# Kernel tuning notes

Hardware: AMD Instinct MI355X
Metric: run time of the kernel (lower is better)

## Reference

```python
import jax, jax.numpy as jnp
import numpy as np

EMBED_DIM = 768
NUM_HEADS = 12
HEAD_DIM = EMBED_DIM // NUM_HEADS
SCALE = HEAD_DIM ** -0.5


def setup_inputs() -> dict:
    key = jax.random.key(0)
    ks = jax.random.split(key, 9)
    s = EMBED_DIM ** -0.5
    x = jax.random.normal(ks[0], (16, 1024, EMBED_DIM), dtype=jnp.float32)
    Wq = jax.random.normal(ks[1], (EMBED_DIM, EMBED_DIM), dtype=jnp.float32) * s
    bq = jax.random.normal(ks[2], (EMBED_DIM,), dtype=jnp.float32) * 0.01
    Wk = jax.random.normal(ks[3], (EMBED_DIM, EMBED_DIM), dtype=jnp.float32) * s
    bk = jax.random.normal(ks[4], (EMBED_DIM,), dtype=jnp.float32) * 0.01
    Wv = jax.random.normal(ks[5], (EMBED_DIM, EMBED_DIM), dtype=jnp.float32) * s
    bv = jax.random.normal(ks[6], (EMBED_DIM,), dtype=jnp.float32) * 0.01
    Wo = jax.random.normal(ks[7], (EMBED_DIM, EMBED_DIM), dtype=jnp.float32) * s
    bo = jax.random.normal(ks[8], (EMBED_DIM,), dtype=jnp.float32) * 0.01
    return {"x": x, "Wq": Wq, "bq": bq, "Wk": Wk, "bk": bk,
            "Wv": Wv, "bv": bv, "Wo": Wo, "bo": bo}


def _split_heads(t):
    # [b, n, h*d] -> [b, h, n, d]
    b, n, _ = t.shape
    return t.reshape(b, n, NUM_HEADS, HEAD_DIM).transpose(0, 2, 1, 3)


def reference(x, Wq, bq, Wk, bk, Wv, bv, Wo, bo):
    # Linear projections (torch Linear: y = x @ W.T + b; W here stored as [out,in])
    Q = _split_heads(x @ Wq.T + bq)
    K = _split_heads(x @ Wk.T + bk)
    V = _split_heads(x @ Wv.T + bv)
    attn = jnp.einsum('bhid,bhjd->bhij', Q, K) * SCALE
    attention = jax.nn.softmax(attn, axis=-1)
    out = jnp.einsum('bhij,bhjd->bhid', attention, V)
    b, h, n, d = out.shape
    out = out.transpose(0, 2, 1, 3).reshape(b, n, h * d)
    return out @ Wo.T + bo
```

## Files before the change

### kernel.cpp

```cpp
#include <hip/hip_runtime.h>

typedef __attribute__((ext_vector_type(8))) short bf16x8;
typedef __attribute__((ext_vector_type(4))) float f32x4;

#define EMBED  768
#define NHEADS 12
#define HDIM   64
#define SEQ    1024
#define BATCH  16
#define MTOT   (BATCH * SEQ)
#define SCALE  0.125f
#define MSHIFT 11.0f
#define SEXP   0.18033688011112042f
#define MEXP   15.869645544856504f

__device__ __forceinline__ unsigned short f2bf(float f) {
  unsigned u = __float_as_uint(f);
  u += 0x7fffu + ((u >> 16) & 1u);
  return (unsigned short)(u >> 16);
}

__device__ __forceinline__ unsigned cvtpk(float lo, float hi) {
  unsigned r;
  asm("v_cvt_pk_bf16_f32 %0, %1, %2" : "=v"(r) : "v"(lo), "v"(hi));
  return r;
}

__device__ __forceinline__ float exp2v(float x) {
  return __builtin_amdgcn_exp2f(x);
}

__device__ __forceinline__ void gld_lds16(const unsigned short* g, unsigned short* l) {
  __builtin_amdgcn_global_load_lds(
      (const __attribute__((address_space(1))) unsigned int*)g,
      (__attribute__((address_space(3))) unsigned int*)l, 16, 0, 0);
}

__global__ void cvt_kernel(const float* __restrict__ in,
                           unsigned short* __restrict__ out, int n) {
  int i = (blockIdx.x * blockDim.x + threadIdx.x) * 4;
  if (i >= n) return;
  float4 v = *(const float4*)(in + i);
  ushort4 o;
  o.x = f2bf(v.x); o.y = f2bf(v.y); o.z = f2bf(v.z); o.w = f2bf(v.w);
  *(ushort4*)(out + i) = o;
}

__global__ void cvt4_kernel(const float* __restrict__ a, const float* __restrict__ b,
                            const float* __restrict__ c, const float* __restrict__ d,
                            unsigned short* __restrict__ oa, unsigned short* __restrict__ ob,
                            unsigned short* __restrict__ oc, unsigned short* __restrict__ od,
                            int n) {
  const int sel = blockIdx.y;
  const float* in = (sel == 0) ? a : (sel == 1) ? b : (sel == 2) ? c : d;
  unsigned short* out = (sel == 0) ? oa : (sel == 1) ? ob : (sel == 2) ? oc : od;
  int i = (blockIdx.x * blockDim.x + threadIdx.x) * 4;
  if (i >= n) return;
  float4 v = *(const float4*)(in + i);
  ushort4 o;
  o.x = f2bf(v.x); o.y = f2bf(v.y); o.z = f2bf(v.z); o.w = f2bf(v.w);
  *(ushort4*)(out + i) = o;
}

__global__ __launch_bounds__(256)
void gemm_qkv(const unsigned short* __restrict__ A,
              const unsigned short* __restrict__ Wq, const unsigned short* __restrict__ Wk,
              const unsigned short* __restrict__ Wv,
              const float* __restrict__ bq, const float* __restrict__ bk,
              const float* __restrict__ bv,
              unsigned short* __restrict__ outq, unsigned short* __restrict__ outk,
              unsigned short* __restrict__ outv) {
  __shared__ unsigned short sA[2 * 128 * 32];
  __shared__ unsigned short sB[2 * 128 * 32];
  const int sel = blockIdx.y / 6;
  const int n0  = (blockIdx.y % 6) * 128;
  const unsigned short* W = (sel == 0) ? Wq : (sel == 1) ? Wk : Wv;
  const float* bias       = (sel == 0) ? bq : (sel == 1) ? bk : bv;

  const int tid  = threadIdx.x;
  const int w    = tid >> 6;
  const int lane = tid & 63;
  const int quad = lane >> 4;
  const int l16  = lane & 15;
  const int mw   = (w & 1) * 64;
  const int nw   = (w >> 1) * 64;
  const int m0   = blockIdx.x * 128;

  const int srow = lane >> 2;
  const int scol = (lane & 3) * 8;
  const unsigned short* Ag0 = A + (size_t)(m0 + w * 16 + srow) * EMBED + scol;
  const unsigned short* Ag1 = Ag0 + (size_t)64 * EMBED;
  const unsigned short* Wg0 = W + (size_t)(n0 + w * 16 + srow) * EMBED + scol;
  const unsigned short* Wg1 = Wg0 + (size_t)64 * EMBED;
  unsigned short* lA0 = sA + w * 16 * 32;
  unsigned short* lA1 = lA0 + 64 * 32;
  unsigned short* lB0 = sB + w * 16 * 32;
  unsigned short* lB1 = lB0 + 64 * 32;

  f32x4 acc[4][4];
#pragma unroll
  for (int i = 0; i < 4; ++i)
#pragma unroll
    for (int j = 0; j < 4; ++j) acc[i][j] = (f32x4){0.f, 0.f, 0.f, 0.f};

  for (int k0 = 0; k0 < EMBED; k0 += 64) {
    __syncthreads();
#pragma unroll
    for (int c = 0; c < 2; ++c) {
      gld_lds16(Ag0 + k0 + c * 32, lA0 + c * 4096);
      gld_lds16(Ag1 + k0 + c * 32, lA1 + c * 4096);
      gld_lds16(Wg0 + k0 + c * 32, lB0 + c * 4096);
      gld_lds16(Wg1 + k0 + c * 32, lB1 + c * 4096);
    }
    __syncthreads();

#pragma unroll
    for (int c = 0; c < 2; ++c) {
      bf16x8 af[4], bfr[4];
#pragma unroll
      for (int i = 0; i < 4; ++i)
        af[i] = *(const bf16x8*)&sA[c * 4096 + (mw + i * 16 + l16) * 32 + quad * 8];
#pragma unroll
      for (int j = 0; j < 4; ++j)
        bfr[j] = *(const bf16x8*)&sB[c * 4096 + (nw + j * 16 + l16) * 32 + quad * 8];
#pragma unroll
      for (int i = 0; i < 4; ++i)
#pragma unroll
        for (int j = 0; j < 4; ++j)
          acc[i][j] = __builtin_amdgcn_mfma_f32_16x16x32_bf16(af[i], bfr[j], acc[i][j], 0, 0, 0);
    }
  }

  if (sel < 2) {
    unsigned short* o = (sel == 0) ? outq : outk;
#pragma unroll
    for (int j = 0; j < 4; ++j) {
      const int col = n0 + nw + j * 16 + l16;
      const float bval = bias[col];
#pragma unroll
      for (int i = 0; i < 4; ++i)
#pragma unroll
        for (int r = 0; r < 4; ++r) {
          const int row = m0 + mw + i * 16 + quad * 4 + r;
          o[(size_t)row * EMBED + col] = f2bf(acc[i][j][r] + bval);
        }
    }
  } else {
    __syncthreads();
    unsigned short* tV = (w < 2) ? (sA + w * 1536) : (sB + (w - 2) * 1536);
    const int n_base = n0 + nw;
    const int hh     = n_base >> 6;
    const int m_base = m0 + mw;
    const int bidx   = m_base >> 10;
    const int seq_b  = m_base & 1023;
    unsigned short* Vout = outv + ((size_t)(bidx * NHEADS + hh)) * HDIM * SEQ;
    float bvv[4];
#pragma unroll
    for (int j = 0; j < 4; ++j) bvv[j] = bias[n_base + j * 16 + l16];
#pragma unroll
    for (int i = 0; i < 4; ++i) {
#pragma unroll
      for (int j = 0; j < 4; ++j) {
        uint2 pk;
        pk.x = cvtpk(acc[i][j][0] + bvv[j], acc[i][j][1] + bvv[j]);
        pk.y = cvtpk(acc[i][j][2] + bvv[j], acc[i][j][3] + bvv[j]);
        *(uint2*)&tV[(j * 16 + l16) * 24 + quad * 4] = pk;
      }
      bf16x8 v0 = *(const bf16x8*)&tV[lane * 24 + 0];
      bf16x8 v1 = *(const bf16x8*)&tV[lane * 24 + 8];
      unsigned short* dst = Vout + (size_t)lane * SEQ + seq_b + i * 16;
      *(bf16x8*)(dst)     = v0;
      *(bf16x8*)(dst + 8) = v1;
    }
  }
}

__global__ __launch_bounds__(256)
void gemm_out(const unsigned short* __restrict__ A,
              const unsigned short* __restrict__ W,
              const float* __restrict__ bias,
              float* __restrict__ out) {
  __shared__ unsigned short sA[2 * 128 * 32];
  __shared__ unsigned short sB[2 * 128 * 32];
  const int tid  = threadIdx.x;
  const int w    = tid >> 6;
  const int lane = tid & 63;
  const int quad = lane >> 4;
  const int l16  = lane & 15;
  const int mw   = (w & 1) * 64;
  const int nw   = (w >> 1) * 64;
  const int m0   = blockIdx.x * 128;
  const int n0   = blockIdx.y * 128;

  const int srow = lane >> 2;
  const int scol = (lane & 3) * 8;
  const unsigned short* Ag0 = A + (size_t)(m0 + w * 16 + srow) * EMBED + scol;
  const unsigned short* Ag1 = Ag0 + (size_t)64 * EMBED;
  const unsigned short* Wg0 = W + (size_t)(n0 + w * 16 + srow) * EMBED + scol;
  const unsigned short* Wg1 = Wg0 + (size_t)64 * EMBED;
  unsigned short* lA0 = sA + w * 16 * 32;
  unsigned short* lA1 = lA0 + 64 * 32;
  unsigned short* lB0 = sB + w * 16 * 32;
  unsigned short* lB1 = lB0 + 64 * 32;

  f32x4 acc[4][4];
#pragma unroll
  for (int i = 0; i < 4; ++i)
#pragma unroll
    for (int j = 0; j < 4; ++j) acc[i][j] = (f32x4){0.f, 0.f, 0.f, 0.f};

  for (int k0 = 0; k0 < EMBED; k0 += 64) {
    __syncthreads();
#pragma unroll
    for (int c = 0; c < 2; ++c) {
      gld_lds16(Ag0 + k0 + c * 32, lA0 + c * 4096);
      gld_lds16(Ag1 + k0 + c * 32, lA1 + c * 4096);
      gld_lds16(Wg0 + k0 + c * 32, lB0 + c * 4096);
      gld_lds16(Wg1 + k0 + c * 32, lB1 + c * 4096);
    }
    __syncthreads();

#pragma unroll
    for (int c = 0; c < 2; ++c) {
      bf16x8 af[4], bfr[4];
#pragma unroll
      for (int i = 0; i < 4; ++i)
        af[i] = *(const bf16x8*)&sA[c * 4096 + (mw + i * 16 + l16) * 32 + quad * 8];
#pragma unroll
      for (int j = 0; j < 4; ++j)
        bfr[j] = *(const bf16x8*)&sB[c * 4096 + (nw + j * 16 + l16) * 32 + quad * 8];
#pragma unroll
      for (int i = 0; i < 4; ++i)
#pragma unroll
        for (int j = 0; j < 4; ++j)
          acc[i][j] = __builtin_amdgcn_mfma_f32_16x16x32_bf16(af[i], bfr[j], acc[i][j], 0, 0, 0);
    }
  }

#pragma unroll
  for (int j = 0; j < 4; ++j) {
    const int col = n0 + nw + j * 16 + l16;
    const float bval = bias[col];
#pragma unroll
    for (int i = 0; i < 4; ++i)
#pragma unroll
      for (int r = 0; r < 4; ++r) {
        const int row = m0 + mw + i * 16 + quad * 4 + r;
        out[(size_t)row * EMBED + col] = acc[i][j][r] + bval;
      }
  }
}

__global__ __launch_bounds__(256)
void attn_kernel(const unsigned short* __restrict__ Q,
                 const unsigned short* __restrict__ K,
                 const unsigned short* __restrict__ VT,
                 unsigned short* __restrict__ O) {
  const int bid = blockIdx.x;
  const int xcd = bid & 7;
  const int s8  = bid >> 3;
  const int bh  = xcd * 24 + (s8 >> 3);
  const int qt  = s8 & 7;
  const int b   = bh / NHEADS;
  const int h   = bh - b * NHEADS;
  const int w    = threadIdx.x >> 6;
  const int lane = threadIdx.x & 63;
  const int quad = lane >> 4;
  const int l16  = lane & 15;
  const int q0   = qt * 128 + w * 32;

  __shared__ unsigned short sK[2][64][32];
  __shared__ unsigned short sV[2][64][32];
  __shared__ __align__(16) unsigned short PT[4][2][16][72];

  bf16x8 bq[2][2];
#pragma unroll
  for (int u = 0; u < 2; ++u) {
    const unsigned short* Qp = Q + (size_t)(b * SEQ + q0 + u * 16 + l16) * EMBED + h * HDIM;
    bq[u][0] = *(const bf16x8*)(Qp + quad * 8);
    bq[u][1] = *(const bf16x8*)(Qp + 32 + quad * 8);
  }

  const int srow = lane >> 2;
  const int scol = (((lane & 3) ^ ((srow >> 1) & 3)) * 8);
  const int qsw  = ((quad ^ ((l16 >> 1) & 3)) * 8);
  const unsigned short* Kg = K + (size_t)(b * SEQ) * EMBED + h * HDIM;
  const unsigned short* Vg = VT + ((size_t)(b * NHEADS + h)) * HDIM * SEQ;

  float l_acc[2] = {0.f, 0.f};
  f32x4 oT[2][4];
#pragma unroll
  for (int u = 0; u < 2; ++u)
#pragma unroll
    for (int t = 0; t < 4; ++t) oT[u][t] = (f32x4){0.f, 0.f, 0.f, 0.f};

  for (int j0 = 0; j0 < SEQ; j0 += 64) {
    __syncthreads();
#pragma unroll
    for (int c = 0; c < 2; ++c) {
      gld_lds16(Kg + (size_t)(j0 + w * 16 + srow) * EMBED + c * 32 + scol, &sK[c][w * 16][0]);
      gld_lds16(Vg + (size_t)(w * 16 + srow) * SEQ + j0 + c * 32 + scol,   &sV[c][w * 16][0]);
    }
    __syncthreads();

    f32x4 sT[2][4];
#pragma unroll
    for (int u = 0; u < 2; ++u)
#pragma unroll
      for (int t = 0; t < 4; ++t) sT[u][t] = (f32x4){0.f, 0.f, 0.f, 0.f};
#pragma unroll
    for (int t = 0; t < 4; ++t) {
      bf16x8 ak0 = *(const bf16x8*)&sK[0][t * 16 + l16][qsw];
      bf16x8 ak1 = *(const bf16x8*)&sK[1][t * 16 + l16][qsw];
#pragma unroll
      for (int u = 0; u < 2; ++u) {
        sT[u][t] = __builtin_amdgcn_mfma_f32_16x16x32_bf16(ak0, bq[u][0], sT[u][t], 0, 0, 0);
        sT[u][t] = __builtin_amdgcn_mfma_f32_16x16x32_bf16(ak1, bq[u][1], sT[u][t], 0, 0, 0);
      }
    }

#pragma unroll
    for (int u = 0; u < 2; ++u) {
#pragma unroll
      for (int t = 0; t < 4; ++t) {
        const float p0 = exp2v(fmaf(sT[u][t][0], SEXP, -MEXP));
        const float p1 = exp2v(fmaf(sT[u][t][1], SEXP, -MEXP));
        const float p2 = exp2v(fmaf(sT[u][t][2], SEXP, -MEXP));
        const float p3 = exp2v(fmaf(sT[u][t][3], SEXP, -MEXP));
        l_acc[u] += (p0 + p1) + (p2 + p3);
        uint2 pk;
        pk.x = cvtpk(p0, p1);
        pk.y = cvtpk(p2, p3);
        *(uint2*)&PT[w][u][l16][t * 16 + quad * 4] = pk;
      }
    }

#pragma unroll
    for (int c = 0; c < 2; ++c) {
      bf16x8 bp0 = *(const bf16x8*)&PT[w][0][l16][c * 32 + quad * 8];
      bf16x8 bp1 = *(const bf16x8*)&PT[w][1][l16][c * 32 + quad * 8];
#pragma unroll
      for (int t = 0; t < 4; ++t) {
        bf16x8 av = *(const bf16x8*)&sV[c][t * 16 + l16][qsw];
        oT[0][t] = __builtin_amdgcn_mfma_f32_16x16x32_bf16(av, bp0, oT[0][t], 0, 0, 0);
        oT[1][t] = __builtin_amdgcn_mfma_f32_16x16x32_bf16(av, bp1, oT[1][t], 0, 0, 0);
      }
    }
  }

#pragma unroll
  for (int u = 0; u < 2; ++u) {
    float l = l_acc[u];
    l += __shfl_xor(l, 16, 64);
    l += __shfl_xor(l, 32, 64);
    const float invl = 1.f / l;
    unsigned short* Orow = O + (size_t)(b * SEQ + q0 + u * 16 + l16) * EMBED + h * HDIM;
#pragma unroll
    for (int t = 0; t < 4; ++t) {
      uint2 pk;
      pk.x = cvtpk(oT[u][t][0] * invl, oT[u][t][1] * invl);
      pk.y = cvtpk(oT[u][t][2] * invl, oT[u][t][3] * invl);
      *(uint2*)(Orow + t * 16 + quad * 4) = pk;
    }
  }
}

extern "C" void kernel_launch(void* const* d_in, const int* in_sizes, int n_in,
                              void* d_out, int out_size, void* d_ws, size_t ws_size,
                              hipStream_t stream) {
  const float* x  = (const float*)d_in[0];
  const float* Wq = (const float*)d_in[1];
  const float* bq = (const float*)d_in[2];
  const float* Wk = (const float*)d_in[3];
  const float* bk = (const float*)d_in[4];
  const float* Wv = (const float*)d_in[5];
  const float* bv = (const float*)d_in[6];
  const float* Wo = (const float*)d_in[7];
  const float* bo = (const float*)d_in[8];

  unsigned short* xb  = (unsigned short*)d_ws;
  unsigned short* qb  = xb  + (size_t)MTOT * EMBED;
  unsigned short* kb  = qb  + (size_t)MTOT * EMBED;
  unsigned short* vtb = kb  + (size_t)MTOT * EMBED;
  unsigned short* ob  = vtb + (size_t)MTOT * EMBED;
  unsigned short* wqb = ob  + (size_t)MTOT * EMBED;
  unsigned short* wkb = wqb + (size_t)EMBED * EMBED;
  unsigned short* wvb = wkb + (size_t)EMBED * EMBED;
  unsigned short* wob = wvb + (size_t)EMBED * EMBED;

  const int nx = MTOT * EMBED;
  const int nw = EMBED * EMBED;
  cvt_kernel<<<dim3(nx / 4 / 256), 256, 0, stream>>>(x, xb, nx);
  cvt4_kernel<<<dim3(nw / 4 / 256, 4), 256, 0, stream>>>(Wq, Wk, Wv, Wo,
                                                         wqb, wkb, wvb, wob, nw);

  gemm_qkv<<<dim3(MTOT / 128, 18), 256, 0, stream>>>(xb, wqb, wkb, wvb,
                                                     bq, bk, bv, qb, kb, vtb);

  attn_kernel<<<dim3(SEQ / 128 * NHEADS * BATCH), 256, 0, stream>>>(qb, kb, vtb, ob);

  gemm_out<<<dim3(MTOT / 128, EMBED / 128), 256, 0, stream>>>(ob, wob, bo, (float*)d_out);
}
```

Measured before the change: 315.3 us.

## Double-buffer LDS staging in GEMMs and attention, merge conversion kernels

Adds double-buffered LDS tiles to gemm_qkv, gemm_out and the attention kernel. The next K tile's global-to-LDS loads are issued before computing on the current tile, leaving one barrier per iteration instead of two, so load latency can overlap MFMA work. It also merges the x and weight bf16 conversion kernels into one launch and packs the Q/K epilogue conversion with cvt_pk. The cost is doubled LDS footprint, which may lower occupancy. There is also a possible race: the loads for the next buffer are issued without waiting on the earlier async global_load_lds writes.

```diff
diff --git a/kernel.cpp b/kernel.cpp
--- a/kernel.cpp
+++ b/kernel.cpp
@@ -36,30 +36,28 @@
       (__attribute__((address_space(3))) unsigned int*)l, 16, 0, 0);
 }
 
-__global__ void cvt_kernel(const float* __restrict__ in,
-                           unsigned short* __restrict__ out, int n) {
+__global__ void cvt_all(const float* __restrict__ x,
+                        const float* __restrict__ wa, const float* __restrict__ wb,
+                        const float* __restrict__ wc, const float* __restrict__ wd,
+                        unsigned short* __restrict__ xo,
+                        unsigned short* __restrict__ oa, unsigned short* __restrict__ ob,
+                        unsigned short* __restrict__ oc, unsigned short* __restrict__ od) {
+  const int NX = MTOT * EMBED;
+  const int NW = EMBED * EMBED;
   int i = (blockIdx.x * blockDim.x + threadIdx.x) * 4;
-  if (i >= n) return;
-  float4 v = *(const float4*)(in + i);
+  const float* in; unsigned short* out; int off;
+  if (i < NX) { in = x; out = xo; off = i; }
+  else {
+    int k = i - NX;
+    int sel = k / NW;
+    off = k - sel * NW;
+    in  = (sel == 0) ? wa : (sel == 1) ? wb : (sel == 2) ? wc : wd;
+    out = (sel == 0) ? oa : (sel == 1) ? ob : (sel == 2) ? oc : od;
+  }
+  float4 v = *(const float4*)(in + off);
   ushort4 o;
   o.x = f2bf(v.x); o.y = f2bf(v.y); o.z = f2bf(v.z); o.w = f2bf(v.w);
-  *(ushort4*)(out + i) = o;
-}
-
-__global__ void cvt4_kernel(const float* __restrict__ a, const float* __restrict__ b,
-                            const float* __restrict__ c, const float* __restrict__ d,
-                            unsigned short* __restrict__ oa, unsigned short* __restrict__ ob,
-                            unsigned short* __restrict__ oc, unsigned short* __restrict__ od,
-                            int n) {
-  const int sel = blockIdx.y;
-  const float* in = (sel == 0) ? a : (sel == 1) ? b : (sel == 2) ? c : d;
-  unsigned short* out = (sel == 0) ? oa : (sel == 1) ? ob : (sel == 2) ? oc : od;
-  int i = (blockIdx.x * blockDim.x + threadIdx.x) * 4;
-  if (i >= n) return;
-  float4 v = *(const float4*)(in + i);
-  ushort4 o;
-  o.x = f2bf(v.x); o.y = f2bf(v.y); o.z = f2bf(v.z); o.w = f2bf(v.w);
-  *(ushort4*)(out + i) = o;
+  *(ushort4*)(out + off) = o;
 }
 
 __global__ __launch_bounds__(256)
@@ -70,8 +68,8 @@
               const float* __restrict__ bv,
               unsigned short* __restrict__ outq, unsigned short* __restrict__ outk,
               unsigned short* __restrict__ outv) {
-  __shared__ unsigned short sA[2 * 128 * 32];
-  __shared__ unsigned short sB[2 * 128 * 32];
+  __shared__ unsigned short sA[2][2 * 128 * 32];
+  __shared__ unsigned short sB[2][2 * 128 * 32];
   const int sel = blockIdx.y / 6;
   const int n0  = (blockIdx.y % 6) * 128;
   const unsigned short* W = (sel == 0) ? Wq : (sel == 1) ? Wk : Wv;
@@ -92,10 +90,7 @@
   const unsigned short* Ag1 = Ag0 + (size_t)64 * EMBED;
   const unsigned short* Wg0 = W + (size_t)(n0 + w * 16 + srow) * EMBED + scol;
   const unsigned short* Wg1 = Wg0 + (size_t)64 * EMBED;
-  unsigned short* lA0 = sA + w * 16 * 32;
-  unsigned short* lA1 = lA0 + 64 * 32;
-  unsigned short* lB0 = sB + w * 16 * 32;
-  unsigned short* lB1 = lB0 + 64 * 32;
+  const int lofs = w * 16 * 32;
 
   f32x4 acc[4][4];
 #pragma unroll
@@ -103,33 +98,41 @@
 #pragma unroll
     for (int j = 0; j < 4; ++j) acc[i][j] = (f32x4){0.f, 0.f, 0.f, 0.f};
 
-  for (int k0 = 0; k0 < EMBED; k0 += 64) {
-    __syncthreads();
-#pragma unroll
-    for (int c = 0; c < 2; ++c) {
-      gld_lds16(Ag0 + k0 + c * 32, lA0 + c * 4096);
-      gld_lds16(Ag1 + k0 + c * 32, lA1 + c * 4096);
-      gld_lds16(Wg0 + k0 + c * 32, lB0 + c * 4096);
-      gld_lds16(Wg1 + k0 + c * 32, lB1 + c * 4096);
-    }
-    __syncthreads();
-
+  auto STAGE = [&](int bu, int k0) {
+#pragma unroll
+    for (int c = 0; c < 2; ++c) {
+      gld_lds16(Ag0 + k0 + c * 32, &sA[bu][lofs + c * 4096]);
+      gld_lds16(Ag1 + k0 + c * 32, &sA[bu][lofs + 64 * 32 + c * 4096]);
+      gld_lds16(Wg0 + k0 + c * 32, &sB[bu][lofs + c * 4096]);
+      gld_lds16(Wg1 + k0 + c * 32, &sB[bu][lofs + 64 * 32 + c * 4096]);
+    }
+  };
+  auto COMPUTE = [&](int cur) {
 #pragma unroll
     for (int c = 0; c < 2; ++c) {
       bf16x8 af[4], bfr[4];
 #pragma unroll
       for (int i = 0; i < 4; ++i)
-        af[i] = *(const bf16x8*)&sA[c * 4096 + (mw + i * 16 + l16) * 32 + quad * 8];
+        af[i] = *(const bf16x8*)&sA[cur][c * 4096 + (mw + i * 16 + l16) * 32 + quad * 8];
 #pragma unroll
       for (int j = 0; j < 4; ++j)
-        bfr[j] = *(const bf16x8*)&sB[c * 4096 + (nw + j * 16 + l16) * 32 + quad * 8];
+        bfr[j] = *(const bf16x8*)&sB[cur][c * 4096 + (nw + j * 16 + l16) * 32 + quad * 8];
 #pragma unroll
       for (int i = 0; i < 4; ++i)
 #pragma unroll
         for (int j = 0; j < 4; ++j)
           acc[i][j] = __builtin_amdgcn_mfma_f32_16x16x32_bf16(af[i], bfr[j], acc[i][j], 0, 0, 0);
     }
-  }
+  };
+
+  STAGE(0, 0);
+  __syncthreads();
+  for (int t = 0; t < 11; ++t) {
+    STAGE((t & 1) ^ 1, (t + 1) * 64);
+    COMPUTE(t & 1);
+    __syncthreads();
+  }
+  COMPUTE(1);
 
   if (sel < 2) {
     unsigned short* o = (sel == 0) ? outq : outk;
@@ -138,16 +141,18 @@
       const int col = n0 + nw + j * 16 + l16;
       const float bval = bias[col];
 #pragma unroll
-      for (int i = 0; i < 4; ++i)
-#pragma unroll
-        for (int r = 0; r < 4; ++r) {
-          const int row = m0 + mw + i * 16 + quad * 4 + r;
-          o[(size_t)row * EMBED + col] = f2bf(acc[i][j][r] + bval);
-        }
+      for (int i = 0; i < 4; ++i) {
+        const unsigned p0 = cvtpk(acc[i][j][0] + bval, acc[i][j][1] + bval);
+        const unsigned p1 = cvtpk(acc[i][j][2] + bval, acc[i][j][3] + bval);
+        const size_t row = (size_t)(m0 + mw + i * 16 + quad * 4);
+        o[row * EMBED + col]       = (unsigned short)p0;
+        o[(row + 1) * EMBED + col] = (unsigned short)(p0 >> 16);
+        o[(row + 2) * EMBED + col] = (unsigned short)p1;
+        o[(row + 3) * EMBED + col] = (unsigned short)(p1 >> 16);
+      }
     }
   } else {
-    __syncthreads();
-    unsigned short* tV = (w < 2) ? (sA + w * 1536) : (sB + (w - 2) * 1536);
+    unsigned short* tV = (w < 2) ? (&sA[0][0] + w * 1536) : (&sB[0][0] + (w - 2) * 1536);
     const int n_base = n0 + nw;
     const int hh     = n_base >> 6;
     const int m_base = m0 + mw;
@@ -180,8 +185,8 @@
               const unsigned short* __restrict__ W,
               const float* __restrict__ bias,
               float* __restrict__ out) {
-  __shared__ unsigned short sA[2 * 128 * 32];
-  __shared__ unsigned short sB[2 * 128 * 32];
+  __shared__ unsigned short sA[2][2 * 128 * 32];
+  __shared__ unsigned short sB[2][2 * 128 * 32];
   const int tid  = threadIdx.x;
   const int w    = tid >> 6;
   const int lane = tid & 63;
@@ -198,10 +203,7 @@
   const unsigned short* Ag1 = Ag0 + (size_t)64 * EMBED;
   const unsigned short* Wg0 = W + (size_t)(n0 + w * 16 + srow) * EMBED + scol;
   const unsigned short* Wg1 = Wg0 + (size_t)64 * EMBED;
-  unsigned short* lA0 = sA + w * 16 * 32;
-  unsigned short* lA1 = lA0 + 64 * 32;
-  unsigned short* lB0 = sB + w * 16 * 32;
-  unsigned short* lB1 = lB0 + 64 * 32;
+  const int lofs = w * 16 * 32;
 
   f32x4 acc[4][4];
 #pragma unroll
@@ -209,33 +211,41 @@
 #pragma unroll
     for (int j = 0; j < 4; ++j) acc[i][j] = (f32x4){0.f, 0.f, 0.f, 0.f};
 
-  for (int k0 = 0; k0 < EMBED; k0 += 64) {
-    __syncthreads();
-#pragma unroll
-    for (int c = 0; c < 2; ++c) {
-      gld_lds16(Ag0 + k0 + c * 32, lA0 + c * 4096);
-      gld_lds16(Ag1 + k0 + c * 32, lA1 + c * 4096);
-      gld_lds16(Wg0 + k0 + c * 32, lB0 + c * 4096);
-      gld_lds16(Wg1 + k0 + c * 32, lB1 + c * 4096);
-    }
-    __syncthreads();
-
+  auto STAGE = [&](int bu, int k0) {
+#pragma unroll
+    for (int c = 0; c < 2; ++c) {
+      gld_lds16(Ag0 + k0 + c * 32, &sA[bu][lofs + c * 4096]);
+      gld_lds16(Ag1 + k0 + c * 32, &sA[bu][lofs + 64 * 32 + c * 4096]);
+      gld_lds16(Wg0 + k0 + c * 32, &sB[bu][lofs + c * 4096]);
+      gld_lds16(Wg1 + k0 + c * 32, &sB[bu][lofs + 64 * 32 + c * 4096]);
+    }
+  };
+  auto COMPUTE = [&](int cur) {
 #pragma unroll
     for (int c = 0; c < 2; ++c) {
       bf16x8 af[4], bfr[4];
 #pragma unroll
       for (int i = 0; i < 4; ++i)
-        af[i] = *(const bf16x8*)&sA[c * 4096 + (mw + i * 16 + l16) * 32 + quad * 8];
+        af[i] = *(const bf16x8*)&sA[cur][c * 4096 + (mw + i * 16 + l16) * 32 + quad * 8];
 #pragma unroll
       for (int j = 0; j < 4; ++j)
-        bfr[j] = *(const bf16x8*)&sB[c * 4096 + (nw + j * 16 + l16) * 32 + quad * 8];
+        bfr[j] = *(const bf16x8*)&sB[cur][c * 4096 + (nw + j * 16 + l16) * 32 + quad * 8];
 #pragma unroll
       for (int i = 0; i < 4; ++i)
 #pragma unroll
         for (int j = 0; j < 4; ++j)
           acc[i][j] = __builtin_amdgcn_mfma_f32_16x16x32_bf16(af[i], bfr[j], acc[i][j], 0, 0, 0);
     }
-  }
+  };
+
+  STAGE(0, 0);
+  __syncthreads();
+  for (int t = 0; t < 11; ++t) {
+    STAGE((t & 1) ^ 1, (t + 1) * 64);
+    COMPUTE(t & 1);
+    __syncthreads();
+  }
+  COMPUTE(1);
 
 #pragma unroll
   for (int j = 0; j < 4; ++j) {
@@ -269,8 +279,8 @@
   const int l16  = lane & 15;
   const int q0   = qt * 128 + w * 32;
 
-  __shared__ unsigned short sK[2][64][32];
-  __shared__ unsigned short sV[2][64][32];
+  __shared__ unsigned short sK[2][2][64][32];
+  __shared__ unsigned short sV[2][2][64][32];
   __shared__ __align__(16) unsigned short PT[4][2][16][72];
 
   bf16x8 bq[2][2];
@@ -294,15 +304,14 @@
 #pragma unroll
     for (int t = 0; t < 4; ++t) oT[u][t] = (f32x4){0.f, 0.f, 0.f, 0.f};
 
-  for (int j0 = 0; j0 < SEQ; j0 += 64) {
-    __syncthreads();
-#pragma unroll
-    for (int c = 0; c < 2; ++c) {
-      gld_lds16(Kg + (size_t)(j0 + w * 16 + srow) * EMBED + c * 32 + scol, &sK[c][w * 16][0]);
-      gld_lds16(Vg + (size_t)(w * 16 + srow) * SEQ + j0 + c * 32 + scol,   &sV[c][w * 16][0]);
-    }
-    __syncthreads();
-
+  auto STAGE = [&](int bu, int j0) {
+#pragma unroll
+    for (int c = 0; c < 2; ++c) {
+      gld_lds16(Kg + (size_t)(j0 + w * 16 + srow) * EMBED + c * 32 + scol, &sK[bu][c][w * 16][0]);
+      gld_lds16(Vg + (size_t)(w * 16 + srow) * SEQ + j0 + c * 32 + scol,   &sV[bu][c][w * 16][0]);
+    }
+  };
+  auto COMPUTE = [&](int cur) {
     f32x4 sT[2][4];
 #pragma unroll
     for (int u = 0; u < 2; ++u)
@@ -310,15 +319,14 @@
       for (int t = 0; t < 4; ++t) sT[u][t] = (f32x4){0.f, 0.f, 0.f, 0.f};
 #pragma unroll
     for (int t = 0; t < 4; ++t) {
-      bf16x8 ak0 = *(const bf16x8*)&sK[0][t * 16 + l16][qsw];
-      bf16x8 ak1 = *(const bf16x8*)&sK[1][t * 16 + l16][qsw];
+      bf16x8 ak0 = *(const bf16x8*)&sK[cur][0][t * 16 + l16][qsw];
+      bf16x8 ak1 = *(const bf16x8*)&sK[cur][1][t * 16 + l16][qsw];
 #pragma unroll
       for (int u = 0; u < 2; ++u) {
         sT[u][t] = __builtin_amdgcn_mfma_f32_16x16x32_bf16(ak0, bq[u][0], sT[u][t], 0, 0, 0);
         sT[u][t] = __builtin_amdgcn_mfma_f32_16x16x32_bf16(ak1, bq[u][1], sT[u][t], 0, 0, 0);
       }
     }
-
 #pragma unroll
     for (int u = 0; u < 2; ++u) {
 #pragma unroll
@@ -334,19 +342,27 @@
         *(uint2*)&PT[w][u][l16][t * 16 + quad * 4] = pk;
       }
     }
-
 #pragma unroll
     for (int c = 0; c < 2; ++c) {
       bf16x8 bp0 = *(const bf16x8*)&PT[w][0][l16][c * 32 + quad * 8];
       bf16x8 bp1 = *(const bf16x8*)&PT[w][1][l16][c * 32 + quad * 8];
 #pragma unroll
       for (int t = 0; t < 4; ++t) {
-        bf16x8 av = *(const bf16x8*)&sV[c][t * 16 + l16][qsw];
+        bf16x8 av = *(const bf16x8*)&sV[cur][c][t * 16 + l16][qsw];
         oT[0][t] = __builtin_amdgcn_mfma_f32_16x16x32_bf16(av, bp0, oT[0][t], 0, 0, 0);
         oT[1][t] = __builtin_amdgcn_mfma_f32_16x16x32_bf16(av, bp1, oT[1][t], 0, 0, 0);
       }
     }
-  }
+  };
+
+  STAGE(0, 0);
+  __syncthreads();
+  for (int jt = 0; jt < 15; ++jt) {
+    STAGE((jt & 1) ^ 1, (jt + 1) * 64);
+    COMPUTE(jt & 1);
+    __syncthreads();
+  }
+  COMPUTE(1);
 
 #pragma unroll
   for (int u = 0; u < 2; ++u) {
@@ -388,11 +404,9 @@
   unsigned short* wvb = wkb + (size_t)EMBED * EMBED;
   unsigned short* wob = wvb + (size_t)EMBED * EMBED;
 
-  const int nx = MTOT * EMBED;
-  const int nw = EMBED * EMBED;
-  cvt_kernel<<<dim3(nx / 4 / 256), 256, 0, stream>>>(x, xb, nx);
-  cvt4_kernel<<<dim3(nw / 4 / 256, 4), 256, 0, stream>>>(Wq, Wk, Wv, Wo,
-                                                         wqb, wkb, wvb, wob, nw);
+  const int ntot = MTOT * EMBED + 4 * EMBED * EMBED;
+  cvt_all<<<dim3(ntot / 4 / 256), 256, 0, stream>>>(x, Wq, Wk, Wv, Wo,
+                                                    xb, wqb, wkb, wvb, wob);
 
   gemm_qkv<<<dim3(MTOT / 128, 18), 256, 0, stream>>>(xb, wqb, wkb, wvb,
                                                      bq, bk, bv, qb, kb, vtb);
```

Result: no change. 315.1 us (-0.1%).
